# Optimization experiments

Measured on AMD Instinct MI355X. Metric: run time of the kernel, lower is better.

Reference implementation:

```python
import jax, jax.numpy as jnp
import numpy as np

INF = 1e9
EPS = 1e-5

def layer_norm(x, g, b):
    mu = jnp.mean(x, axis=-1, keepdims=True)
    var = jnp.mean(jnp.square(x - mu), axis=-1, keepdims=True)
    return (x - mu) * jax.lax.rsqrt(var + EPS) * g + b

def setup_inputs() -> dict:
    key = jax.random.key(0)
    ks = jax.random.split(key, 12)
    B, S, N = 1, 512, 384
    c_in, c_hid, c_z, H = 64, 32, 128, 8
    d = c_hid * H
    sc = lambda fan: 1.0 / np.sqrt(fan)
    return {
        "m": jax.random.normal(ks[0], (B, S, N, c_in), jnp.float32),
        "z": jax.random.normal(ks[1], (B, N, N, c_z), jnp.float32),
        "mask": jnp.ones((B, N, N), jnp.float32),
        "gamma_m": jnp.ones((c_in,), jnp.float32),
        "beta_m": jnp.zeros((c_in,), jnp.float32),
        "gamma_z": jnp.ones((c_z,), jnp.float32),
        "beta_z": jnp.zeros((c_z,), jnp.float32),
        "w_z": jax.random.normal(ks[2], (c_z, H), jnp.float32) * sc(c_z),
        "b_z": jnp.zeros((H,), jnp.float32),
        "w_v": jax.random.normal(ks[3], (c_in, d), jnp.float32) * sc(c_in),
        "b_v": jnp.zeros((d,), jnp.float32),
        "w_g": jax.random.normal(ks[4], (c_in, d), jnp.float32) * sc(c_in),
        "b_g": jnp.zeros((d,), jnp.float32),
        "w_o": jax.random.normal(ks[5], (d, c_in), jnp.float32) * sc(d),
        "b_o": jnp.zeros((c_in,), jnp.float32),
    }

def reference(m, z, mask, gamma_m, beta_m, gamma_z, beta_z,
              w_z, b_z, w_v, b_v, w_g, b_g, w_o, b_o):
    B, S, N, c_in = m.shape
    H = w_z.shape[-1]
    C = w_v.shape[-1] // H
    # pair branch: LN -> linear -> [B,H,Nq,Nk] logits + mask bias -> softmax
    zn = layer_norm(z, gamma_z, beta_z)
    logits = jnp.einsum('bqkz,zh->bhqk', zn, w_z) + b_z[None, :, None, None]
    logits = logits + (INF * (mask - 1.0))[:, None, :, :]
    w = jax.nn.softmax(logits, axis=-1)                      # [B,H,Nq,Nk]
    # MSA branch: LN -> value / gate projections
    mn = layer_norm(m, gamma_m, beta_m)
    v = (mn @ w_v + b_v).reshape(B, S, N, H, C)              # [B,S,Nk,H,C]
    o = jnp.einsum('bhqk,bskhc->bsqhc', w, v)                # broadcast over S
    g = jax.nn.sigmoid(mn @ w_g + b_g).reshape(B, S, N, H, C)
    out = (o * g).reshape(B, S, N, H * C) @ w_o + b_o
    return out
```

## Files before the change

kernel.cpp:

```cpp
#include <hip/hip_runtime.h>
#include <hip/hip_bf16.h>

#define INFV 1e9f
#define EPSV 1e-5f

typedef unsigned short u16;
typedef unsigned int u32;
typedef __attribute__((ext_vector_type(8))) short short8;
typedef __attribute__((ext_vector_type(4))) float float4v;

__device__ __forceinline__ u16 f2us(float f) {
    u32 v;
    __builtin_memcpy(&v, &f, 4);
    u32 r = v + 0x7fffu + ((v >> 16) & 1u);
    return (u16)(r >> 16);
}

__device__ __forceinline__ float wred_sum(float x) {
    #pragma unroll
    for (int o = 32; o; o >>= 1) x += __shfl_xor(x, o);
    return x;
}
__device__ __forceinline__ float wred_max(float x) {
    #pragma unroll
    for (int o = 32; o; o >>= 1) x = fmaxf(x, __shfl_xor(x, o));
    return x;
}

__global__ __launch_bounds__(256) void k_prep_ln(
    const float* __restrict__ m, const float* __restrict__ gm, const float* __restrict__ bm,
    u16* __restrict__ mn,
    const float* __restrict__ wv, const float* __restrict__ wg,
    const float* __restrict__ wo, const float* __restrict__ wz,
    u16* __restrict__ wv_t, u16* __restrict__ wg_t,
    u16* __restrict__ wo_t, u16* __restrict__ wzT)
{
    if (blockIdx.x < 12288) {
        const int tid  = threadIdx.x;
        const int wid  = tid >> 6;
        const int lane = tid & 63;
        const int rloc = lane >> 4;
        const int c4   = (lane & 15) * 4;
        const int row  = blockIdx.x * 16 + wid * 4 + rloc;
        const float4 x = *(const float4*)(m + (size_t)row * 64 + c4);
        float s1 = x.x + x.y + x.z + x.w;
        float s2 = x.x * x.x + x.y * x.y + x.z * x.z + x.w * x.w;
        #pragma unroll
        for (int o = 8; o; o >>= 1) { s1 += __shfl_xor(s1, o); s2 += __shfl_xor(s2, o); }
        const float mean = s1 * (1.0f / 64.0f);
        const float var  = s2 * (1.0f / 64.0f) - mean * mean;
        const float rs   = rsqrtf(var + EPSV);
        const float4 g = *(const float4*)(gm + c4);
        const float4 b = *(const float4*)(bm + c4);
        uint2 pk;
        pk.x = (u32)f2us((x.x - mean) * rs * g.x + b.x) | ((u32)f2us((x.y - mean) * rs * g.y + b.y) << 16);
        pk.y = (u32)f2us((x.z - mean) * rs * g.z + b.z) | ((u32)f2us((x.w - mean) * rs * g.w + b.w) << 16);
        *(uint2*)(mn + (size_t)row * 64 + c4) = pk;
    } else {
        const int i = (blockIdx.x - 12288) * 256 + threadIdx.x;
        if (i < 16384) {
            const int n = i >> 6, k = i & 63;
            wv_t[i] = f2us(wv[(size_t)k * 256 + n]);
        } else if (i < 32768) {
            const int j = i - 16384, n = j >> 6, k = j & 63;
            wg_t[j] = f2us(wg[(size_t)k * 256 + n]);
        } else if (i < 49152) {
            const int j = i - 32768, n = j >> 8, k = j & 255;
            wo_t[j] = f2us(wo[(size_t)k * 64 + n]);
        } else if (i < 51200) {
            const int j = i - 49152, n = j >> 7, k = j & 127;
            wzT[j] = (n < 8) ? f2us(wz[(size_t)k * 8 + n]) : (u16)0;
        }
    }
}

__global__ __launch_bounds__(256) void k_logits2(
    const float* __restrict__ z, const float* __restrict__ mask,
    const float* __restrict__ gz, const float* __restrict__ bz,
    const u16* __restrict__ wzT, const float* __restrict__ bzb,
    float* __restrict__ wbuf)
{
    const int tid   = threadIdx.x;
    const int wid   = tid >> 6;
    const int lane  = tid & 63;
    const int lrow  = lane & 15;
    const int lkg   = lane >> 4;
    const int pair0 = (blockIdx.x * 4 + wid) * 16;

    float x[4][8];
    float s1 = 0.0f, s2 = 0.0f;
    #pragma unroll
    for (int ks = 0; ks < 4; ks++) {
        const float4* zp = (const float4*)(z + (size_t)(pair0 + lrow) * 128 + ks * 32 + lkg * 8);
        const float4 a = zp[0], b = zp[1];
        x[ks][0] = a.x; x[ks][1] = a.y; x[ks][2] = a.z; x[ks][3] = a.w;
        x[ks][4] = b.x; x[ks][5] = b.y; x[ks][6] = b.z; x[ks][7] = b.w;
        #pragma unroll
        for (int j = 0; j < 8; j++) { s1 += x[ks][j]; s2 += x[ks][j] * x[ks][j]; }
    }
    s1 += __shfl_xor(s1, 16); s1 += __shfl_xor(s1, 32);
    s2 += __shfl_xor(s2, 16); s2 += __shfl_xor(s2, 32);
    const float mean = s1 * (1.0f / 128.0f);
    const float var  = s2 * (1.0f / 128.0f) - mean * mean;
    const float rs   = rsqrtf(var + EPSV);

    float4v acc = (float4v){0.f, 0.f, 0.f, 0.f};
    #pragma unroll
    for (int ks = 0; ks < 4; ks++) {
        const int c0 = ks * 32 + lkg * 8;
        const float4 g0 = *(const float4*)(gz + c0);
        const float4 g1 = *(const float4*)(gz + c0 + 4);
        const float4 b0 = *(const float4*)(bz + c0);
        const float4 b1 = *(const float4*)(bz + c0 + 4);
        const float gv[8] = {g0.x, g0.y, g0.z, g0.w, g1.x, g1.y, g1.z, g1.w};
        const float bvv[8] = {b0.x, b0.y, b0.z, b0.w, b1.x, b1.y, b1.z, b1.w};
        short8 afr;
        #pragma unroll
        for (int j = 0; j < 8; j++)
            afr[j] = (short)f2us((x[ks][j] - mean) * rs * gv[j] + bvv[j]);
        const short8 bfr = *(const short8*)(wzT + (size_t)lrow * 128 + c0);
        acc = __builtin_amdgcn_mfma_f32_16x16x32_bf16(afr, bfr, acc, 0, 0, 0);
    }
    if (lrow < 8) {
        const float bzv = bzb[lrow];
        #pragma unroll
        for (int r = 0; r < 4; r++) {
            const int p = pair0 + lkg * 4 + r;
            const float mb = INFV * (mask[p] - 1.0f);
            wbuf[(size_t)lrow * 147456 + p] = acc[r] + bzv + mb;
        }
    }
}

__global__ __launch_bounds__(256) void k_softmax(
    const float* __restrict__ wbuf, u16* __restrict__ wb16)
{
    const int r = blockIdx.x * 4 + (threadIdx.x >> 6);
    const int lane = threadIdx.x & 63;
    const float* base = wbuf + (size_t)r * 384;
    float v[6];
    float mx = -1e30f;
    #pragma unroll
    for (int j = 0; j < 6; j++) {
        v[j] = base[lane + j * 64];
        mx = fmaxf(mx, v[j]);
    }
    mx = wred_max(mx);
    float s = 0.0f;
    #pragma unroll
    for (int j = 0; j < 6; j++) {
        v[j] = __expf(v[j] - mx);
        s += v[j];
    }
    s = wred_sum(s);
    const float inv = 1.0f / s;
    u16* ob = wb16 + (size_t)r * 384;
    #pragma unroll
    for (int j = 0; j < 6; j++) ob[lane + j * 64] = f2us(v[j] * inv);
}

__global__ __launch_bounds__(256, 2) void k_fused4(
    const u16* __restrict__ mn,
    const float* __restrict__ bv, const float* __restrict__ bg, const float* __restrict__ bo,
    const u16* __restrict__ wv_t, const u16* __restrict__ wg_t, const u16* __restrict__ wo_t,
    const u16* __restrict__ wb16, float* __restrict__ out)
{
    __shared__ __align__(16) char smem[67584];
    u16* vtt = (u16*)smem;
    u16* og  = (u16*)smem;

    const int tid  = threadIdx.x;
    const int wid  = tid >> 6;
    const int lane = tid & 63;
    const int lrow = lane & 15;
    const int lkg  = lane >> 4;
    const int s    = blockIdx.y;
    const int q0   = blockIdx.x * 128;

    const int vmt  = wid & 1;
    const int vnt0 = (wid >> 1) * 8;

    float4v oacc[32];
    #pragma unroll
    for (int mt = 0; mt < 2; mt++)
        #pragma unroll
        for (int nt = 0; nt < 16; nt++) {
            const float b = bv[nt * 16 + lrow];
            oacc[mt * 16 + nt] = (float4v){b, b, b, b};
        }

    for (int kt = 0; kt < 12; kt++) {
        const int k0 = kt * 32;
        float4v vacc[8];
        #pragma unroll
        for (int nt = 0; nt < 8; nt++) vacc[nt] = (float4v){0.f, 0.f, 0.f, 0.f};
        const u16* mnk = mn + ((size_t)s * 384 + k0 + vmt * 16 + lrow) * 64;
        #pragma unroll
        for (int ks = 0; ks < 2; ks++) {
            const short8 a = *(const short8*)(mnk + ks * 32 + lkg * 8);
            #pragma unroll
            for (int nt = 0; nt < 8; nt++) {
                const short8 b = *(const short8*)(wv_t + (size_t)((vnt0 + nt) * 16 + lrow) * 64 + ks * 32 + lkg * 8);
                vacc[nt] = __builtin_amdgcn_mfma_f32_16x16x32_bf16(a, b, vacc[nt], 0, 0, 0);
            }
        }
        u16* vb = vtt + (size_t)(kt & 1) * 8192;
        const int kg8 = vmt * 2 + (lkg >> 1);
        const int ko  = (lkg & 1) * 4;
        #pragma unroll
        for (int nt = 0; nt < 8; nt++) {
            uint2 pk;
            pk.x = (u32)f2us(vacc[nt][0]) | ((u32)f2us(vacc[nt][1]) << 16);
            pk.y = (u32)f2us(vacc[nt][2]) | ((u32)f2us(vacc[nt][3]) << 16);
            *(uint2*)&vb[((size_t)kg8 * 256 + (vnt0 + nt) * 16 + lrow) * 8 + ko] = pk;
        }
        __syncthreads();

        short8 ah[2][8];
        #pragma unroll
        for (int mt = 0; mt < 2; mt++)
            #pragma unroll
            for (int h = 0; h < 8; h++)
                ah[mt][h] = *(const short8*)(wb16 + (size_t)h * 147456
                              + (size_t)(q0 + wid * 32 + mt * 16 + lrow) * 384 + k0 + lkg * 8);
        #pragma unroll
        for (int nt = 0; nt < 16; nt++) {
            const short8 b = *(const short8*)&vb[((size_t)lkg * 256 + nt * 16 + lrow) * 8];
            oacc[nt]      = __builtin_amdgcn_mfma_f32_16x16x32_bf16(ah[0][nt >> 1], b, oacc[nt], 0, 0, 0);
            oacc[16 + nt] = __builtin_amdgcn_mfma_f32_16x16x32_bf16(ah[1][nt >> 1], b, oacc[16 + nt], 0, 0, 0);
        }
    }
    __syncthreads();

    #pragma unroll
    for (int mt = 0; mt < 2; mt++) {
        const u16* mnq = mn + ((size_t)s * 384 + q0 + wid * 32 + mt * 16 + lrow) * 64;
        const short8 a0 = *(const short8*)(mnq + lkg * 8);
        const short8 a1 = *(const short8*)(mnq + 32 + lkg * 8);
        #pragma unroll
        for (int nt = 0; nt < 16; nt++) {
            const float bgv = bg[nt * 16 + lrow];
            float4v gacc = (float4v){bgv, bgv, bgv, bgv};
            const short8 b0 = *(const short8*)(wg_t + (size_t)(nt * 16 + lrow) * 64 + lkg * 8);
            const short8 b1 = *(const short8*)(wg_t + (size_t)(nt * 16 + lrow) * 64 + 32 + lkg * 8);
            gacc = __builtin_amdgcn_mfma_f32_16x16x32_bf16(a0, b0, gacc, 0, 0, 0);
            gacc = __builtin_amdgcn_mfma_f32_16x16x32_bf16(a1, b1, gacc, 0, 0, 0);
            #pragma unroll
            for (int r = 0; r < 4; r++) {
                const float sg = 1.0f / (1.0f + __expf(-gacc[r]));
                og[(size_t)(wid * 32 + mt * 16 + lkg * 4 + r) * 264 + nt * 16 + lrow]
                    = f2us(oacc[mt * 16 + nt][r] * sg);
            }
        }
    }
    __syncthreads();

    #pragma unroll
    for (int mt = 0; mt < 2; mt++) {
        short8 af[8];
        #pragma unroll
        for (int ks = 0; ks < 8; ks++)
            af[ks] = *(const short8*)&og[(size_t)(wid * 32 + mt * 16 + lrow) * 264 + ks * 32 + lkg * 8];
        #pragma unroll
        for (int nt = 0; nt < 4; nt++) {
            const float bov = bo[nt * 16 + lrow];
            float4v fac = (float4v){bov, bov, bov, bov};
            #pragma unroll
            for (int ks = 0; ks < 8; ks++) {
                const short8 b = *(const short8*)(wo_t + (size_t)(nt * 16 + lrow) * 256 + ks * 32 + lkg * 8);
                fac = __builtin_amdgcn_mfma_f32_16x16x32_bf16(af[ks], b, fac, 0, 0, 0);
            }
            #pragma unroll
            for (int r = 0; r < 4; r++)
                out[((size_t)s * 384 + q0 + wid * 32 + mt * 16 + lkg * 4 + r) * 64 + nt * 16 + lrow]
                    = fac[r];
        }
    }
}

extern "C" void kernel_launch(void* const* d_in, const int* in_sizes, int n_in,
                              void* d_out, int out_size, void* d_ws, size_t ws_size,
                              hipStream_t stream) {
    const float* m    = (const float*)d_in[0];
    const float* z    = (const float*)d_in[1];
    const float* mask = (const float*)d_in[2];
    const float* gm   = (const float*)d_in[3];
    const float* bm   = (const float*)d_in[4];
    const float* gz   = (const float*)d_in[5];
    const float* bz   = (const float*)d_in[6];
    const float* wz   = (const float*)d_in[7];
    const float* bzb  = (const float*)d_in[8];
    const float* wv   = (const float*)d_in[9];
    const float* bv   = (const float*)d_in[10];
    const float* wg   = (const float*)d_in[11];
    const float* bg   = (const float*)d_in[12];
    const float* wo   = (const float*)d_in[13];
    const float* bo   = (const float*)d_in[14];
    float* out = (float*)d_out;

    char* ws = (char*)d_ws;
    float* wbuf = (float*)ws;
    u16*  wb16  = (u16*)(ws + 4718592);
    u16*  mn    = (u16*)(ws + 7077888);
    u16*  wv_t  = (u16*)(ws + 32243712);
    u16*  wg_t  = (u16*)(ws + 32276480);
    u16*  wo_t  = (u16*)(ws + 32309248);
    u16*  wzT   = (u16*)(ws + 32342016);

    k_prep_ln<<<12488, 256, 0, stream>>>(m, gm, bm, mn, wv, wg, wo, wz, wv_t, wg_t, wo_t, wzT);
    k_logits2<<<2304,  256, 0, stream>>>(z, mask, gz, bz, wzT, bzb, wbuf);
    k_softmax<<<768,   256, 0, stream>>>(wbuf, wb16);
    k_fused4 <<<dim3(3, 512), 256, 0, stream>>>(mn, bv, bg, bo, wv_t, wg_t, wo_t, wb16, out);
}
```

Baseline: 462.6 us.

## Software-pipeline V projection tile one step ahead of attention accumulation

The fused kernel now computes the first V tile before the loop, then inside each k-step it prefetches the next mn rows, runs the attention MFMAs on the current shared-memory buffer, and computes the next V tile into the other double buffer. This leaves one barrier per iteration, and the next tile's global loads and V MFMAs can overlap with the current tile's work. In exchange it raises register pressure, since the prefetched operands and the V accumulators are live alongside the 32 output accumulators, which could cause spills at the two-waves launch bound.

New measurement: 480.2 us. +3.8%, slower.

```diff
diff --git a/kernel.cpp b/kernel.cpp
--- a/kernel.cpp
+++ b/kernel.cpp
@@ -159,7 +159,7 @@
     for (int j = 0; j < 6; j++) ob[lane + j * 64] = f2us(v[j] * inv);
 }
 
-__global__ __launch_bounds__(256, 2) void k_fused4(
+__global__ __launch_bounds__(256, 2) void k_fused5(
     const u16* __restrict__ mn,
     const float* __restrict__ bv, const float* __restrict__ bg, const float* __restrict__ bo,
     const u16* __restrict__ wv_t, const u16* __restrict__ wg_t, const u16* __restrict__ wo_t,
@@ -179,6 +179,8 @@
 
     const int vmt  = wid & 1;
     const int vnt0 = (wid >> 1) * 8;
+    const int kg8  = vmt * 2 + (lkg >> 1);
+    const int ko   = (lkg & 1) * 4;
 
     float4v oacc[32];
     #pragma unroll
@@ -189,12 +191,11 @@
             oacc[mt * 16 + nt] = (float4v){b, b, b, b};
         }
 
-    for (int kt = 0; kt < 12; kt++) {
-        const int k0 = kt * 32;
+    {
+        const u16* mnk = mn + ((size_t)s * 384 + vmt * 16 + lrow) * 64;
         float4v vacc[8];
         #pragma unroll
         for (int nt = 0; nt < 8; nt++) vacc[nt] = (float4v){0.f, 0.f, 0.f, 0.f};
-        const u16* mnk = mn + ((size_t)s * 384 + k0 + vmt * 16 + lrow) * 64;
         #pragma unroll
         for (int ks = 0; ks < 2; ks++) {
             const short8 a = *(const short8*)(mnk + ks * 32 + lkg * 8);
@@ -204,18 +205,28 @@
                 vacc[nt] = __builtin_amdgcn_mfma_f32_16x16x32_bf16(a, b, vacc[nt], 0, 0, 0);
             }
         }
-        u16* vb = vtt + (size_t)(kt & 1) * 8192;
-        const int kg8 = vmt * 2 + (lkg >> 1);
-        const int ko  = (lkg & 1) * 4;
         #pragma unroll
         for (int nt = 0; nt < 8; nt++) {
             uint2 pk;
             pk.x = (u32)f2us(vacc[nt][0]) | ((u32)f2us(vacc[nt][1]) << 16);
             pk.y = (u32)f2us(vacc[nt][2]) | ((u32)f2us(vacc[nt][3]) << 16);
-            *(uint2*)&vb[((size_t)kg8 * 256 + (vnt0 + nt) * 16 + lrow) * 8 + ko] = pk;
-        }
-        __syncthreads();
-
+            *(uint2*)&vtt[((size_t)kg8 * 256 + (vnt0 + nt) * 16 + lrow) * 8 + ko] = pk;
+        }
+    }
+    __syncthreads();
+
+    for (int kt = 0; kt < 12; kt++) {
+        const int cur = kt & 1;
+        const int k0  = kt * 32;
+
+        short8 an0, an1;
+        if (kt < 11) {
+            const u16* mnk = mn + ((size_t)s * 384 + k0 + 32 + vmt * 16 + lrow) * 64;
+            an0 = *(const short8*)(mnk + lkg * 8);
+            an1 = *(const short8*)(mnk + 32 + lkg * 8);
+        }
+
+        const u16* vb = vtt + (size_t)cur * 8192;
         short8 ah[2][8];
         #pragma unroll
         for (int mt = 0; mt < 2; mt++)
@@ -229,8 +240,32 @@
             oacc[nt]      = __builtin_amdgcn_mfma_f32_16x16x32_bf16(ah[0][nt >> 1], b, oacc[nt], 0, 0, 0);
             oacc[16 + nt] = __builtin_amdgcn_mfma_f32_16x16x32_bf16(ah[1][nt >> 1], b, oacc[16 + nt], 0, 0, 0);
         }
-    }
-    __syncthreads();
+
+        if (kt < 11) {
+            float4v vacc[8];
+            #pragma unroll
+            for (int nt = 0; nt < 8; nt++) vacc[nt] = (float4v){0.f, 0.f, 0.f, 0.f};
+            #pragma unroll
+            for (int nt = 0; nt < 8; nt++) {
+                const short8 b0 = *(const short8*)(wv_t + (size_t)((vnt0 + nt) * 16 + lrow) * 64 + lkg * 8);
+                vacc[nt] = __builtin_amdgcn_mfma_f32_16x16x32_bf16(an0, b0, vacc[nt], 0, 0, 0);
+            }
+            #pragma unroll
+            for (int nt = 0; nt < 8; nt++) {
+                const short8 b1 = *(const short8*)(wv_t + (size_t)((vnt0 + nt) * 16 + lrow) * 64 + 32 + lkg * 8);
+                vacc[nt] = __builtin_amdgcn_mfma_f32_16x16x32_bf16(an1, b1, vacc[nt], 0, 0, 0);
+            }
+            u16* vbn = vtt + (size_t)(cur ^ 1) * 8192;
+            #pragma unroll
+            for (int nt = 0; nt < 8; nt++) {
+                uint2 pk;
+                pk.x = (u32)f2us(vacc[nt][0]) | ((u32)f2us(vacc[nt][1]) << 16);
+                pk.y = (u32)f2us(vacc[nt][2]) | ((u32)f2us(vacc[nt][3]) << 16);
+                *(uint2*)&vbn[((size_t)kg8 * 256 + (vnt0 + nt) * 16 + lrow) * 8 + ko] = pk;
+            }
+        }
+        __syncthreads();
+    }
 
     #pragma unroll
     for (int mt = 0; mt < 2; mt++) {
@@ -310,5 +345,5 @@
     k_prep_ln<<<12488, 256, 0, stream>>>(m, gm, bm, mn, wv, wg, wo, wz, wv_t, wg_t, wo_t, wzT);
     k_logits2<<<2304,  256, 0, stream>>>(z, mask, gz, bz, wzT, bzb, wbuf);
     k_softmax<<<768,   256, 0, stream>>>(wbuf, wb16);
-    k_fused4 <<<dim3(3, 512), 256, 0, stream>>>(mn, bv, bg, bo, wv_t, wg_t, wo_t, wb16, out);
-}
+    k_fused5 <<<dim3(3, 512), 256, 0, stream>>>(mn, bv, bg, bo, wv_t, wg_t, wo_t, wb16, out);
+}
```

## Precompute transposed V in a separate kernel and stream it in the fused attention kernel

Applied to the files above, without the earlier changes.

Adds k_vT, which computes the value projection for every (s, key) pair and stores it transposed in bf16 in workspace. A new k_fused6 kernel then reads V^T straight from global memory instead of recomputing it into shared memory, keeps the attention accumulators in registers, and uses shared memory only for the gated output before the output projection. Blocks are remapped so that consecutive S indices land on the same XCD, to improve L2 locality of V^T. The new path runs only when the workspace is large enough (about 98 MB of extra V^T traffic) and otherwise falls back to k_fused4.

New measurement: 548.3 us. 1.19x slower.

```diff
diff --git a/kernel.cpp b/kernel.cpp
--- a/kernel.cpp
+++ b/kernel.cpp
@@ -74,6 +74,35 @@
     }
 }
 
+__global__ __launch_bounds__(256) void k_vT(
+    const u16* __restrict__ mn, const u16* __restrict__ wv_t, u16* __restrict__ vT)
+{
+    const int tid  = threadIdx.x;
+    const int wid  = tid >> 6;
+    const int lane = tid & 63;
+    const int lrow = lane & 15;
+    const int lkg  = lane >> 4;
+    const int s    = blockIdx.y;
+    const int k0   = blockIdx.x * 64 + wid * 16;
+
+    const u16* mnk = mn + ((size_t)s * 384 + k0 + lrow) * 64;
+    const short8 a0 = *(const short8*)(mnk + lkg * 8);
+    const short8 a1 = *(const short8*)(mnk + 32 + lkg * 8);
+
+    #pragma unroll
+    for (int nt = 0; nt < 16; nt++) {
+        const short8 b0 = *(const short8*)(wv_t + (size_t)(nt * 16 + lrow) * 64 + lkg * 8);
+        const short8 b1 = *(const short8*)(wv_t + (size_t)(nt * 16 + lrow) * 64 + 32 + lkg * 8);
+        float4v acc = (float4v){0.f, 0.f, 0.f, 0.f};
+        acc = __builtin_amdgcn_mfma_f32_16x16x32_bf16(a0, b0, acc, 0, 0, 0);
+        acc = __builtin_amdgcn_mfma_f32_16x16x32_bf16(a1, b1, acc, 0, 0, 0);
+        uint2 pk;
+        pk.x = (u32)f2us(acc[0]) | ((u32)f2us(acc[1]) << 16);
+        pk.y = (u32)f2us(acc[2]) | ((u32)f2us(acc[3]) << 16);
+        *(uint2*)(vT + (size_t)(s * 256 + nt * 16 + lrow) * 384 + k0 + lkg * 4) = pk;
+    }
+}
+
 __global__ __launch_bounds__(256) void k_logits2(
     const float* __restrict__ z, const float* __restrict__ mask,
     const float* __restrict__ gz, const float* __restrict__ bz,
@@ -157,6 +186,110 @@
     u16* ob = wb16 + (size_t)r * 384;
     #pragma unroll
     for (int j = 0; j < 6; j++) ob[lane + j * 64] = f2us(v[j] * inv);
+}
+
+__global__ __launch_bounds__(256, 2) void k_fused6(
+    const u16* __restrict__ mn, const u16* __restrict__ vT,
+    const float* __restrict__ bv, const float* __restrict__ bg, const float* __restrict__ bo,
+    const u16* __restrict__ wg_t, const u16* __restrict__ wo_t,
+    const u16* __restrict__ wb16, float* __restrict__ out)
+{
+    __shared__ __align__(16) u16 og[128 * 264];
+
+    const int tid  = threadIdx.x;
+    const int wid  = tid >> 6;
+    const int lane = tid & 63;
+    const int lrow = lane & 15;
+    const int lkg  = lane >> 4;
+
+    const int bid  = blockIdx.x;
+    const int xcd  = bid & 7;
+    const int slot = bid >> 3;
+    const int sdiv = slot / 3;
+    const int q0   = (slot - sdiv * 3) * 128;
+    const int s    = sdiv * 8 + xcd;
+
+    float4v oacc[32];
+    #pragma unroll
+    for (int mt = 0; mt < 2; mt++)
+        #pragma unroll
+        for (int nt = 0; nt < 16; nt++) {
+            const float b = bv[nt * 16 + lrow];
+            oacc[mt * 16 + nt] = (float4v){b, b, b, b};
+        }
+
+    const u16* vTs = vT + (size_t)s * 98304;
+    const u16* wbq = wb16 + (size_t)(q0 + wid * 32 + lrow) * 384;
+
+    for (int kt = 0; kt < 12; kt++) {
+        const int k0 = kt * 32;
+        short8 ah[2][8];
+        #pragma unroll
+        for (int mt = 0; mt < 2; mt++)
+            #pragma unroll
+            for (int h = 0; h < 8; h++)
+                ah[mt][h] = *(const short8*)(wbq + (size_t)h * 147456 + (size_t)mt * 16 * 384 + k0 + lkg * 8);
+        #pragma unroll
+        for (int nt = 0; nt < 16; nt++) {
+            const short8 b = *(const short8*)(vTs + (size_t)(nt * 16 + lrow) * 384 + k0 + lkg * 8);
+            oacc[nt]      = __builtin_amdgcn_mfma_f32_16x16x32_bf16(ah[0][nt >> 1], b, oacc[nt], 0, 0, 0);
+            oacc[16 + nt] = __builtin_amdgcn_mfma_f32_16x16x32_bf16(ah[1][nt >> 1], b, oacc[16 + nt], 0, 0, 0);
+        }
+    }
+
+    {
+        const u16* mnq = mn + ((size_t)s * 384 + q0 + wid * 32 + lrow) * 64;
+        const short8 a00 = *(const short8*)(mnq + lkg * 8);
+        const short8 a01 = *(const short8*)(mnq + 32 + lkg * 8);
+        const short8 a10 = *(const short8*)(mnq + 16 * 64 + lkg * 8);
+        const short8 a11 = *(const short8*)(mnq + 16 * 64 + 32 + lkg * 8);
+        #pragma unroll
+        for (int nt = 0; nt < 16; nt++) {
+            const float bgv = bg[nt * 16 + lrow];
+            const short8 b0 = *(const short8*)(wg_t + (size_t)(nt * 16 + lrow) * 64 + lkg * 8);
+            const short8 b1 = *(const short8*)(wg_t + (size_t)(nt * 16 + lrow) * 64 + 32 + lkg * 8);
+            float4v g0 = (float4v){bgv, bgv, bgv, bgv};
+            float4v g1 = (float4v){bgv, bgv, bgv, bgv};
+            g0 = __builtin_amdgcn_mfma_f32_16x16x32_bf16(a00, b0, g0, 0, 0, 0);
+            g0 = __builtin_amdgcn_mfma_f32_16x16x32_bf16(a01, b1, g0, 0, 0, 0);
+            g1 = __builtin_amdgcn_mfma_f32_16x16x32_bf16(a10, b0, g1, 0, 0, 0);
+            g1 = __builtin_amdgcn_mfma_f32_16x16x32_bf16(a11, b1, g1, 0, 0, 0);
+            #pragma unroll
+            for (int r = 0; r < 4; r++) {
+                const float s0 = 1.0f / (1.0f + __expf(-g0[r]));
+                const float s1 = 1.0f / (1.0f + __expf(-g1[r]));
+                og[(size_t)(wid * 32 + lkg * 4 + r) * 264 + nt * 16 + lrow]      = f2us(oacc[nt][r] * s0);
+                og[(size_t)(wid * 32 + 16 + lkg * 4 + r) * 264 + nt * 16 + lrow] = f2us(oacc[16 + nt][r] * s1);
+            }
+        }
+    }
+    __syncthreads();
+
+    {
+        short8 af0[8], af1[8];
+        #pragma unroll
+        for (int ks = 0; ks < 8; ks++) {
+            af0[ks] = *(const short8*)&og[(size_t)(wid * 32 + lrow) * 264 + ks * 32 + lkg * 8];
+            af1[ks] = *(const short8*)&og[(size_t)(wid * 32 + 16 + lrow) * 264 + ks * 32 + lkg * 8];
+        }
+        #pragma unroll
+        for (int nt = 0; nt < 4; nt++) {
+            const float bov = bo[nt * 16 + lrow];
+            float4v f0 = (float4v){bov, bov, bov, bov};
+            float4v f1 = (float4v){bov, bov, bov, bov};
+            #pragma unroll
+            for (int ks = 0; ks < 8; ks++) {
+                const short8 b = *(const short8*)(wo_t + (size_t)(nt * 16 + lrow) * 256 + ks * 32 + lkg * 8);
+                f0 = __builtin_amdgcn_mfma_f32_16x16x32_bf16(af0[ks], b, f0, 0, 0, 0);
+                f1 = __builtin_amdgcn_mfma_f32_16x16x32_bf16(af1[ks], b, f1, 0, 0, 0);
+            }
+            #pragma unroll
+            for (int r = 0; r < 4; r++) {
+                out[((size_t)s * 384 + q0 + wid * 32 + lkg * 4 + r) * 64 + nt * 16 + lrow]      = f0[r];
+                out[((size_t)s * 384 + q0 + wid * 32 + 16 + lkg * 4 + r) * 64 + nt * 16 + lrow] = f1[r];
+            }
+        }
+    }
 }
 
 __global__ __launch_bounds__(256, 2) void k_fused4(
@@ -306,9 +439,17 @@
     u16*  wg_t  = (u16*)(ws + 32276480);
     u16*  wo_t  = (u16*)(ws + 32309248);
     u16*  wzT   = (u16*)(ws + 32342016);
+    u16*  vT    = (u16*)(ws + 32346112);
+
+    const bool big = ws_size >= 133009408ull;
 
     k_prep_ln<<<12488, 256, 0, stream>>>(m, gm, bm, mn, wv, wg, wo, wz, wv_t, wg_t, wo_t, wzT);
-    k_logits2<<<2304,  256, 0, stream>>>(z, mask, gz, bz, wzT, bzb, wbuf);
-    k_softmax<<<768,   256, 0, stream>>>(wbuf, wb16);
-    k_fused4 <<<dim3(3, 512), 256, 0, stream>>>(mn, bv, bg, bo, wv_t, wg_t, wo_t, wb16, out);
-}
+    if (big)
+        k_vT<<<dim3(6, 512), 256, 0, stream>>>(mn, wv_t, vT);
+    k_logits2<<<2304, 256, 0, stream>>>(z, mask, gz, bz, wzT, bzb, wbuf);
+    k_softmax<<<768,  256, 0, stream>>>(wbuf, wb16);
+    if (big)
+        k_fused6<<<1536, 256, 0, stream>>>(mn, vT, bv, bg, bo, wg_t, wo_t, wb16, out);
+    else
+        k_fused4<<<dim3(3, 512), 256, 0, stream>>>(mn, bv, bg, bo, wv_t, wg_t, wo_t, wb16, out);
+}
```
